# Performance work log

Hardware: AMD Instinct MI355X
Metric: run time of the kernel (lower is better)

Reference implementation:

```python
import jax, jax.numpy as jnp
import numpy as np

N_CORES = 64
N_QUBITS = 1024
QEMB = 256
N_EDGES = 448
BATCH = 512
NN_DIMS = (256, 512, 512, 256)


def setup_inputs() -> dict:
    key = jax.random.key(0)
    ks = jax.random.split(key, 12)
    inp = {
        "core_allocs": jax.random.randint(ks[0], (BATCH, N_QUBITS), 0, N_CORES, dtype=jnp.int32),
        "qubit_embs": jax.random.normal(ks[1], (N_QUBITS, QEMB), dtype=jnp.float32),
        "dummy_qubit_emb": jax.random.normal(ks[2], (QEMB,), dtype=jnp.float32),
        "edge_index": jax.random.randint(ks[3], (2, N_EDGES), 0, N_CORES, dtype=jnp.int32),
        "edge_weight": jax.random.uniform(ks[4], (N_EDGES,), dtype=jnp.float32),
        "W1": jax.random.normal(ks[5], (NN_DIMS[0], NN_DIMS[1]), dtype=jnp.float32) * 0.05,
        "b1": jax.random.normal(ks[6], (NN_DIMS[1],), dtype=jnp.float32) * 0.05,
        "W2": jax.random.normal(ks[7], (NN_DIMS[1], NN_DIMS[2]), dtype=jnp.float32) * 0.05,
        "b2": jax.random.normal(ks[8], (NN_DIMS[2],), dtype=jnp.float32) * 0.05,
        "W3": jax.random.normal(ks[9], (NN_DIMS[2], NN_DIMS[3]), dtype=jnp.float32) * 0.05,
        "b3": jax.random.normal(ks[10], (NN_DIMS[3],), dtype=jnp.float32) * 0.05,
    }
    return inp


def _gcn_norm(edge_index, edge_weight):
    # PyG gcn_norm: add self loops (weight 1), symmetric D^{-1/2} A D^{-1/2}.
    self_idx = jnp.arange(N_CORES, dtype=edge_index.dtype)
    row = jnp.concatenate([edge_index[0], self_idx])
    col = jnp.concatenate([edge_index[1], self_idx])
    w = jnp.concatenate([edge_weight, jnp.ones((N_CORES,), edge_weight.dtype)])
    deg = jax.ops.segment_sum(w, col, num_segments=N_CORES)  # degree at targets
    dinv = jnp.where(deg > 0, deg ** -0.5, 0.0)
    norm = dinv[row] * w * dinv[col]
    return row, col, norm


def reference(core_allocs, qubit_embs, dummy_qubit_emb, edge_index, edge_weight,
              W1, b1, W2, b2, W3, b3):
    # ---- unmixedCoreEmbs, vectorized: per-core max over assigned qubit embs,
    # dummy emb always included (cores never at capacity) ----
    def pool(alloc):  # alloc: [n_qubits] -> [n_cores, qemb]
        seg = jax.ops.segment_max(qubit_embs, alloc, num_segments=N_CORES)
        return jnp.maximum(seg, dummy_qubit_emb)  # also fixes -inf empty cores

    x = jax.vmap(pool)(core_allocs)  # [B, n_cores, qemb]

    # ---- GCNConv stack (same graph replicated per batch element) ----
    row, col, norm = _gcn_norm(edge_index, edge_weight)

    def gcn_layer(h, W, b):
        hw = h @ W  # [B, C, d_out]
        msg = hw[:, row, :] * norm[None, :, None]  # gather sources, scale
        agg = jnp.zeros((h.shape[0], N_CORES, W.shape[1]), hw.dtype).at[:, col, :].add(msg)
        return jax.nn.relu(agg + b)

    x = gcn_layer(x, W1, b1)
    x = gcn_layer(x, W2, b2)
    x = gcn_layer(x, W3, b3)
    return x  # [B, n_cores, nn_dims[-1]] (original returns this split per batch element)
```

## Files before the change

kernel.cpp:

```cpp
#include <hip/hip_runtime.h>
#include <type_traits>

typedef __attribute__((ext_vector_type(8))) short short8;
typedef __attribute__((ext_vector_type(4))) short short4v;
typedef __attribute__((ext_vector_type(4))) float f32x4;
typedef unsigned short u16;
typedef unsigned int u32;

#define N_EDGES 448

#define WS_ADJA 0
#define WS_ADJB 4096
#define WS_W1   8192
#define WS_W2   139264
#define WS_W3   401408
#define WS_DUM  532480
#define WS_B1   (WS_DUM + 256)
#define WS_B2   (WS_DUM + 768)
#define WS_B3   (WS_DUM + 1280)
#define WS_QE   534528
#define WS_FLAG 796672

__device__ __forceinline__ float bf2f(u16 v) {
    u32 u = ((u32)v) << 16;
    return __builtin_bit_cast(float, u);
}
__device__ __forceinline__ u16 f2bf(float f) {
    u32 u = __builtin_bit_cast(u32, f);
    u32 r = u + 0x7FFFu + ((u >> 16) & 1u);
    return (u16)(r >> 16);
}
__device__ __forceinline__ float ldf(const void* p, int idx, u32 isf32) {
    return isf32 ? ((const float*)p)[idx] : bf2f(((const u16*)p)[idx]);
}

__global__ __launch_bounds__(512) void prep(
    const int* __restrict__ eidx, const void* __restrict__ ew,
    const void* __restrict__ qembs, const void* __restrict__ dummy,
    const void* __restrict__ W1, const void* __restrict__ b1,
    const void* __restrict__ W2, const void* __restrict__ b2,
    const void* __restrict__ W3, const void* __restrict__ b3,
    u16* __restrict__ ws) {
    const int t = threadIdx.x, bb = blockIdx.x;
    __shared__ u32 s_isf;
    if (t < 64) {
        const u16* qs = (const u16*)qembs;
        int c = 0;
#pragma unroll
        for (int j = 0; j < 4; j++) {
            u16 v = qs[(t * 4 + j) * 2];
            u32 e = (v >> 7) & 0xFF;
            c += (e >= 100 && e <= 134) ? 1 : 0;
        }
#pragma unroll
        for (int off = 32; off > 0; off >>= 1) c += __shfl_down(c, off, 64);
        if (t == 0) s_isf = (c < 128) ? 1u : 0u;
    }
    __syncthreads();
    const u32 isf32 = s_isf;

    if (t < 128) {
        const int bw = bb * 2 + (t >> 6);
        const int tl = t & 63;
        const void* src;
        int N, K32, dst, nt, kk;
        if (bw < 256)      { src = W1; N = 512; K32 = 8;  dst = WS_W1; nt = bw / 8;          kk = bw % 8; }
        else if (bw < 768) { src = W2; N = 512; K32 = 16; dst = WS_W2; nt = (bw - 256) / 16; kk = (bw - 256) % 16; }
        else               { src = W3; N = 256; K32 = 16; dst = WS_W3; nt = (bw - 768) / 16; kk = (bw - 768) % 16; }
        const int col = nt * 16 + (tl & 15);
        const int krow = kk * 32 + (tl >> 4) * 8;
        u16 v[8];
#pragma unroll
        for (int j = 0; j < 8; j++) v[j] = f2bf(ldf(src, (krow + j) * N + col, isf32));
        u16* o = ws + dst + (nt * K32 + kk) * 512 + tl * 8;
#pragma unroll
        for (int j = 0; j < 8; j++) o[j] = v[j];
    }
    if (t >= 256) {
        const int base = bb * 512 + (t - 256) * 2;
        ws[WS_QE + base]     = f2bf(ldf(qembs, base, isf32));
        ws[WS_QE + base + 1] = f2bf(ldf(qembs, base + 1, isf32));
    }
    if (bb == 1) {
#pragma unroll
        for (int j = 0; j < 4; j++) {
            int i = t + j * 512;
            if (i < 1792) {
                float v;
                if (i < 256)       v = ldf(dummy, i, isf32);
                else if (i < 768)  v = ldf(b1, i - 256, isf32);
                else if (i < 1280) v = ldf(b2, i - 768, isf32);
                else               v = ldf(b3, i - 1280, isf32);
                ws[WS_DUM + i] = f2bf(v);
            }
        }
    }
    if (bb == 0) {
        __shared__ float A[4096];
        __shared__ float deg[64];
        __shared__ float dinv[64];
        __shared__ int er[N_EDGES];
        __shared__ int ec[N_EDGES];
        __shared__ float ewf[N_EDGES];
        if (t < N_EDGES) {
            er[t] = eidx[t];
            ec[t] = eidx[N_EDGES + t];
            ewf[t] = ldf(ew, t, isf32);
        }
        if (t < 64) deg[t] = 1.0f;
        for (int i = t; i < 4096; i += 512) A[i] = 0.f;
        __syncthreads();
        if (t < N_EDGES) atomicAdd(&deg[ec[t]], ewf[t]);
        __syncthreads();
        if (t < 64) dinv[t] = 1.0f / sqrtf(deg[t]);
        __syncthreads();
        if (t < N_EDGES) atomicAdd(&A[ec[t] * 64 + er[t]], dinv[er[t]] * ewf[t] * dinv[ec[t]]);
        __syncthreads();
        if (t < 64) A[t * 64 + t] += dinv[t] * dinv[t];
        __syncthreads();
        for (int i = t; i < 4096; i += 512) {
            int chunk = i >> 9, m = (i >> 3) & 63, j = i & 7;
            ws[WS_ADJA + i] = f2bf(A[m * 64 + chunk * 8 + j]);
        }
        for (int i = t; i < 4096; i += 512) {
            int chunk = i >> 9, l = (i >> 3) & 63, j = i & 7;
            int ntc = chunk >> 1, kk = chunk & 1;
            int k = kk * 32 + (l >> 4) * 8 + j;
            int c2 = ntc * 16 + (l & 15);
            ws[WS_ADJB + i] = f2bf(A[c2 * 64 + k]);
        }
        if (t == 0) *(u32*)(ws + WS_FLAG) = isf32;
    }
}

__global__ __launch_bounds__(1024, 8) void fused(
    const int* __restrict__ allocs, const u16* __restrict__ ws,
    void* __restrict__ out) {

    __shared__ __align__(16) u16 H[64 * 512];

    const int t = threadIdx.x, bb = blockIdx.x;
    const int wave = t >> 6, lane = t & 63, quad = lane >> 4, nl = lane & 15;

    {
        int* LIST = (int*)H + 8192;
        int* CNT  = LIST + 1024;
        int* SST  = CNT + 64;
        int* WOF  = SST + 64;
        if (t < 64) CNT[t] = 0;
        __syncthreads();
        const int myc = allocs[bb * 1024 + t];
        atomicAdd(&CNT[myc], 1);
        __syncthreads();
        if (t < 64) {
            int v = CNT[t], s = v;
#pragma unroll
            for (int off = 1; off < 64; off <<= 1) {
                int u = __shfl_up(s, off, 64);
                if (t >= off) s += u;
            }
            SST[t] = s - v;
            WOF[t] = s - v;
        }
        __syncthreads();
        {
            int pos = atomicAdd(&WOF[myc], 1);
            LIST[pos] = t;
        }
        __syncthreads();
        const int half = lane >> 5, sl = lane & 31;
        const u16* wsq = ws + WS_QE;
        for (int i = 0; i < 4; i++) {
            const int c = wave * 4 + i;
            const int L = CNT[c], S = SST[c];
            float vm[8];
#pragma unroll
            for (int k = 0; k < 8; k++) vm[k] = bf2f(ws[WS_DUM + sl * 8 + k]);
            for (int j = half; j < L; j += 2) {
                int q = LIST[S + j];
                uint4 r = *(const uint4*)(wsq + q * 256 + sl * 8);
                vm[0] = fmaxf(vm[0], bf2f((u16)(r.x & 0xffff)));
                vm[1] = fmaxf(vm[1], bf2f((u16)(r.x >> 16)));
                vm[2] = fmaxf(vm[2], bf2f((u16)(r.y & 0xffff)));
                vm[3] = fmaxf(vm[3], bf2f((u16)(r.y >> 16)));
                vm[4] = fmaxf(vm[4], bf2f((u16)(r.z & 0xffff)));
                vm[5] = fmaxf(vm[5], bf2f((u16)(r.z >> 16)));
                vm[6] = fmaxf(vm[6], bf2f((u16)(r.w & 0xffff)));
                vm[7] = fmaxf(vm[7], bf2f((u16)(r.w >> 16)));
            }
            short8 p;
#pragma unroll
            for (int k = 0; k < 8; k++) {
                float o = __shfl_xor(vm[k], 32, 64);
                p[k] = (short)f2bf(fmaxf(vm[k], o));
            }
            if (half == 0) *(short8*)(H + sl * 512 + c * 8) = p;
        }
    }
    __syncthreads();

    auto layerT = [&](auto K32c, const u16* __restrict__ W, const u16* __restrict__ bias) {
        constexpr int K32 = decltype(K32c)::value;
        const int s0 = wave * 2;
        u16* scr = H + (wave * 4 + 2) * 512;
        f32x4 acc[2][4];
#pragma unroll
        for (int s = 0; s < 2; s++)
#pragma unroll
            for (int rt = 0; rt < 4; rt++) acc[s][rt] = f32x4{0.f, 0.f, 0.f, 0.f};
#pragma unroll
        for (int kk = 0; kk < K32; kk++) {
            short8 a[4], bch[2];
#pragma unroll
            for (int rt = 0; rt < 4; rt++)
                a[rt] = *(const short8*)(H + (kk * 4 + quad) * 512 + (rt * 16 + nl) * 8);
#pragma unroll
            for (int s = 0; s < 2; s++)
                bch[s] = *(const short8*)(W + ((s0 + s) * K32 + kk) * 512 + lane * 8);
#pragma unroll
            for (int s = 0; s < 2; s++)
#pragma unroll
                for (int rt = 0; rt < 4; rt++)
                    acc[s][rt] = __builtin_amdgcn_mfma_f32_16x16x32_bf16(a[rt], bch[s], acc[s][rt], 0, 0, 0);
        }
        __syncthreads();
#pragma unroll
        for (int s = 0; s < 2; s++) {
            const int nt = s0 + s;
            f32x4 agg[4];
#pragma unroll
            for (int ntc = 0; ntc < 4; ntc++) agg[ntc] = f32x4{0.f, 0.f, 0.f, 0.f};
#pragma unroll
            for (int h = 0; h < 2; h++) {
#pragma unroll
                for (int r2 = 0; r2 < 2; r2++) {
                    f32x4 v = acc[s][2 * h + r2];
                    short4v p;
#pragma unroll
                    for (int rr = 0; rr < 4; rr++) p[rr] = (short)f2bf(v[rr]);
                    *(short4v*)(scr + nl * 40 + r2 * 16 + quad * 4) = p;
                }
                short8 hwf = *(const short8*)(scr + nl * 40 + quad * 8);
#pragma unroll
                for (int ntc = 0; ntc < 4; ntc++) {
                    short8 adjB = *(const short8*)(ws + WS_ADJB + (ntc * 2 + h) * 512 + lane * 8);
                    agg[ntc] = __builtin_amdgcn_mfma_f32_16x16x32_bf16(hwf, adjB, agg[ntc], 0, 0, 0);
                }
            }
            float bv[4];
#pragma unroll
            for (int rr = 0; rr < 4; rr++) bv[rr] = bf2f(bias[nt * 16 + quad * 4 + rr]);
#pragma unroll
            for (int ntc = 0; ntc < 4; ntc++) {
                short4v p;
#pragma unroll
                for (int rr = 0; rr < 4; rr++)
                    p[rr] = (short)f2bf(fmaxf(agg[ntc][rr] + bv[rr], 0.f));
                *(short4v*)(H + (nt * 2 + (quad >> 1)) * 512 + (ntc * 16 + nl) * 8 + (quad & 1) * 4) = p;
            }
        }
        __syncthreads();
    };

    auto layer3 = [&](const u16* __restrict__ W) {
        const int nt = wave;
        u16* scr = H + 16384 + wave * 640;
        f32x4 acc[4];
#pragma unroll
        for (int rt = 0; rt < 4; rt++) acc[rt] = f32x4{0.f, 0.f, 0.f, 0.f};
#pragma unroll
        for (int kk = 0; kk < 16; kk++) {
            short8 a[4];
#pragma unroll
            for (int rt = 0; rt < 4; rt++)
                a[rt] = *(const short8*)(H + (kk * 4 + quad) * 512 + (rt * 16 + nl) * 8);
            short8 bch = *(const short8*)(W + (nt * 16 + kk) * 512 + lane * 8);
#pragma unroll
            for (int rt = 0; rt < 4; rt++)
                acc[rt] = __builtin_amdgcn_mfma_f32_16x16x32_bf16(a[rt], bch, acc[rt], 0, 0, 0);
        }
        __syncthreads();
#pragma unroll
        for (int h = 0; h < 2; h++) {
#pragma unroll
            for (int r2 = 0; r2 < 2; r2++) {
                f32x4 v = acc[2 * h + r2];
                short4v p;
#pragma unroll
                for (int rr = 0; rr < 4; rr++) p[rr] = (short)f2bf(v[rr]);
                *(short4v*)(scr + nl * 40 + r2 * 16 + quad * 4) = p;
            }
            short8 hwf = *(const short8*)(scr + nl * 40 + quad * 8);
            *(short8*)(H + (nt * 2 + h) * 512 + lane * 8) = hwf;
        }
        __syncthreads();
    };

    auto finalOut = [&]() {
        const u32 isf32 = *(const u32*)(ws + WS_FLAG);
        const int rt2 = wave & 3, nt0 = (wave >> 2) * 4;
        short8 aA[2];
#pragma unroll
        for (int h = 0; h < 2; h++)
            aA[h] = *(const short8*)(ws + WS_ADJA + (h * 4 + quad) * 512 + (rt2 * 16 + nl) * 8);
        f32x4 accv[4];
#pragma unroll
        for (int ni = 0; ni < 4; ni++) {
            const int nt = nt0 + ni;
            short8 b0v = *(const short8*)(H + (nt * 2 + 0) * 512 + lane * 8);
            short8 b1v = *(const short8*)(H + (nt * 2 + 1) * 512 + lane * 8);
            f32x4 a = f32x4{0.f, 0.f, 0.f, 0.f};
            a = __builtin_amdgcn_mfma_f32_16x16x32_bf16(aA[0], b0v, a, 0, 0, 0);
            a = __builtin_amdgcn_mfma_f32_16x16x32_bf16(aA[1], b1v, a, 0, 0, 0);
            accv[ni] = a;
        }
        __syncthreads();
        float* Hf = (float*)H;
#pragma unroll
        for (int ni = 0; ni < 4; ni++) {
            const int n = (nt0 + ni) * 16 + nl;
            const float bv = bf2f(ws[WS_B3 + n]);
#pragma unroll
            for (int rr = 0; rr < 4; rr++) {
                const int m2 = rt2 * 16 + quad * 4 + rr;
                Hf[m2 * 256 + n] = fmaxf(accv[ni][rr] + bv, 0.f);
            }
        }
        __syncthreads();
        if (isf32) {
            float4* outv = (float4*)((float*)out + (size_t)bb * 16384);
            const float4* Hv = (const float4*)Hf;
#pragma unroll
            for (int p4 = 0; p4 < 4; p4++) outv[p4 * 1024 + t] = Hv[p4 * 1024 + t];
        } else {
            u16* outu = (u16*)out + (size_t)bb * 16384;
#pragma unroll
            for (int p4 = 0; p4 < 4; p4++) {
                const int idx = (p4 * 1024 + t) * 4;
                float4 v = *(const float4*)(Hf + idx);
                short4v pk;
                pk[0] = (short)f2bf(v.x); pk[1] = (short)f2bf(v.y);
                pk[2] = (short)f2bf(v.z); pk[3] = (short)f2bf(v.w);
                *(short4v*)(outu + idx) = pk;
            }
        }
    };

    layerT(std::integral_constant<int, 8>{},  ws + WS_W1, ws + WS_B1);
    layerT(std::integral_constant<int, 16>{}, ws + WS_W2, ws + WS_B2);
    layer3(ws + WS_W3);
    finalOut();
}

extern "C" void kernel_launch(void* const* d_in, const int* in_sizes, int n_in,
                              void* d_out, int out_size, void* d_ws, size_t ws_size,
                              hipStream_t stream) {
    const int* allocs = (const int*)d_in[0];
    const void* qembs = d_in[1];
    const void* dummy = d_in[2];
    const int* eidx   = (const int*)d_in[3];
    const void* ew    = d_in[4];
    const void* W1 = d_in[5];
    const void* b1 = d_in[6];
    const void* W2 = d_in[7];
    const void* b2 = d_in[8];
    const void* W3 = d_in[9];
    const void* b3 = d_in[10];
    u16* ws = (u16*)d_ws;

    prep<<<512, 512, 0, stream>>>(eidx, ew, qembs, dummy, W1, b1, W2, b2, W3, b3, ws);
    fused<<<512, 1024, 0, stream>>>(allocs, ws, d_out);
}
```

Measured before the change: 173.0 us.

## Halve fused block to 512 threads, doubling per-wave GEMM tiles; use cheaper bf16 rounding

The fused kernel now runs 512 threads per block instead of 1024, and each wave covers twice as many output tiles in every stage: pooling over 8 cores, 4 n-tiles in the first two GCN layers, 2 in layer3, and 8 in the final output. This raises per-wave register reuse of the A fragments loaded from LDS and cuts barrier participants. The price is fewer waves for latency hiding and more accumulator registers. Float-to-bf16 conversion also switches to round-half-up without ties-to-even, which saves a few ALU ops but can differ slightly in rounding.

```diff
diff --git a/kernel.cpp b/kernel.cpp
--- a/kernel.cpp
+++ b/kernel.cpp
@@ -29,6 +29,10 @@
     u32 u = __builtin_bit_cast(u32, f);
     u32 r = u + 0x7FFFu + ((u >> 16) & 1u);
     return (u16)(r >> 16);
+}
+__device__ __forceinline__ u16 f2bf_fast(float f) {
+    u32 u = __builtin_bit_cast(u32, f);
+    return (u16)((u + 0x8000u) >> 16);
 }
 __device__ __forceinline__ float ldf(const void* p, int idx, u32 isf32) {
     return isf32 ? ((const float*)p)[idx] : bf2f(((const u16*)p)[idx]);
@@ -133,7 +137,7 @@
     }
 }
 
-__global__ __launch_bounds__(1024, 8) void fused(
+__global__ __launch_bounds__(512, 4) void fused(
     const int* __restrict__ allocs, const u16* __restrict__ ws,
     void* __restrict__ out) {
 
@@ -149,8 +153,10 @@
         int* WOF  = SST + 64;
         if (t < 64) CNT[t] = 0;
         __syncthreads();
-        const int myc = allocs[bb * 1024 + t];
-        atomicAdd(&CNT[myc], 1);
+        const int c1 = allocs[bb * 1024 + t];
+        const int c2 = allocs[bb * 1024 + 512 + t];
+        atomicAdd(&CNT[c1], 1);
+        atomicAdd(&CNT[c2], 1);
         __syncthreads();
         if (t < 64) {
             int v = CNT[t], s = v;
@@ -164,14 +170,14 @@
         }
         __syncthreads();
         {
-            int pos = atomicAdd(&WOF[myc], 1);
-            LIST[pos] = t;
+            int p1 = atomicAdd(&WOF[c1], 1); LIST[p1] = t;
+            int p2 = atomicAdd(&WOF[c2], 1); LIST[p2] = 512 + t;
         }
         __syncthreads();
         const int half = lane >> 5, sl = lane & 31;
         const u16* wsq = ws + WS_QE;
-        for (int i = 0; i < 4; i++) {
-            const int c = wave * 4 + i;
+        for (int i = 0; i < 8; i++) {
+            const int c = wave * 8 + i;
             const int L = CNT[c], S = SST[c];
             float vm[8];
 #pragma unroll
@@ -192,7 +198,7 @@
 #pragma unroll
             for (int k = 0; k < 8; k++) {
                 float o = __shfl_xor(vm[k], 32, 64);
-                p[k] = (short)f2bf(fmaxf(vm[k], o));
+                p[k] = (short)f2bf_fast(fmaxf(vm[k], o));
             }
             if (half == 0) *(short8*)(H + sl * 512 + c * 8) = p;
         }
@@ -201,31 +207,31 @@
 
     auto layerT = [&](auto K32c, const u16* __restrict__ W, const u16* __restrict__ bias) {
         constexpr int K32 = decltype(K32c)::value;
-        const int s0 = wave * 2;
-        u16* scr = H + (wave * 4 + 2) * 512;
-        f32x4 acc[2][4];
-#pragma unroll
-        for (int s = 0; s < 2; s++)
+        const int s0 = wave * 4;
+        u16* scr = H + (wave * 8 + 6) * 512;
+        f32x4 acc[4][4];
+#pragma unroll
+        for (int s = 0; s < 4; s++)
 #pragma unroll
             for (int rt = 0; rt < 4; rt++) acc[s][rt] = f32x4{0.f, 0.f, 0.f, 0.f};
 #pragma unroll
         for (int kk = 0; kk < K32; kk++) {
-            short8 a[4], bch[2];
+            short8 a[4], bch[4];
 #pragma unroll
             for (int rt = 0; rt < 4; rt++)
                 a[rt] = *(const short8*)(H + (kk * 4 + quad) * 512 + (rt * 16 + nl) * 8);
 #pragma unroll
-            for (int s = 0; s < 2; s++)
+            for (int s = 0; s < 4; s++)
                 bch[s] = *(const short8*)(W + ((s0 + s) * K32 + kk) * 512 + lane * 8);
 #pragma unroll
-            for (int s = 0; s < 2; s++)
+            for (int s = 0; s < 4; s++)
 #pragma unroll
                 for (int rt = 0; rt < 4; rt++)
                     acc[s][rt] = __builtin_amdgcn_mfma_f32_16x16x32_bf16(a[rt], bch[s], acc[s][rt], 0, 0, 0);
         }
         __syncthreads();
 #pragma unroll
-        for (int s = 0; s < 2; s++) {
+        for (int s = 0; s < 4; s++) {
             const int nt = s0 + s;
             f32x4 agg[4];
 #pragma unroll
@@ -237,7 +243,7 @@
                     f32x4 v = acc[s][2 * h + r2];
                     short4v p;
 #pragma unroll
-                    for (int rr = 0; rr < 4; rr++) p[rr] = (short)f2bf(v[rr]);
+                    for (int rr = 0; rr < 4; rr++) p[rr] = (short)f2bf_fast(v[rr]);
                     *(short4v*)(scr + nl * 40 + r2 * 16 + quad * 4) = p;
                 }
                 short8 hwf = *(const short8*)(scr + nl * 40 + quad * 8);
@@ -255,7 +261,7 @@
                 short4v p;
 #pragma unroll
                 for (int rr = 0; rr < 4; rr++)
-                    p[rr] = (short)f2bf(fmaxf(agg[ntc][rr] + bv[rr], 0.f));
+                    p[rr] = (short)f2bf_fast(fmaxf(agg[ntc][rr] + bv[rr], 0.f));
                 *(short4v*)(H + (nt * 2 + (quad >> 1)) * 512 + (ntc * 16 + nl) * 8 + (quad & 1) * 4) = p;
             }
         }
@@ -263,49 +269,59 @@
     };
 
     auto layer3 = [&](const u16* __restrict__ W) {
-        const int nt = wave;
+        const int s0 = wave * 2;
         u16* scr = H + 16384 + wave * 640;
-        f32x4 acc[4];
-#pragma unroll
-        for (int rt = 0; rt < 4; rt++) acc[rt] = f32x4{0.f, 0.f, 0.f, 0.f};
+        f32x4 acc[2][4];
+#pragma unroll
+        for (int s = 0; s < 2; s++)
+#pragma unroll
+            for (int rt = 0; rt < 4; rt++) acc[s][rt] = f32x4{0.f, 0.f, 0.f, 0.f};
 #pragma unroll
         for (int kk = 0; kk < 16; kk++) {
-            short8 a[4];
+            short8 a[4], bch[2];
 #pragma unroll
             for (int rt = 0; rt < 4; rt++)
                 a[rt] = *(const short8*)(H + (kk * 4 + quad) * 512 + (rt * 16 + nl) * 8);
-            short8 bch = *(const short8*)(W + (nt * 16 + kk) * 512 + lane * 8);
-#pragma unroll
-            for (int rt = 0; rt < 4; rt++)
-                acc[rt] = __builtin_amdgcn_mfma_f32_16x16x32_bf16(a[rt], bch, acc[rt], 0, 0, 0);
-        }
-        __syncthreads();
-#pragma unroll
-        for (int h = 0; h < 2; h++) {
-#pragma unroll
-            for (int r2 = 0; r2 < 2; r2++) {
-                f32x4 v = acc[2 * h + r2];
-                short4v p;
-#pragma unroll
-                for (int rr = 0; rr < 4; rr++) p[rr] = (short)f2bf(v[rr]);
-                *(short4v*)(scr + nl * 40 + r2 * 16 + quad * 4) = p;
-            }
-            short8 hwf = *(const short8*)(scr + nl * 40 + quad * 8);
-            *(short8*)(H + (nt * 2 + h) * 512 + lane * 8) = hwf;
+#pragma unroll
+            for (int s = 0; s < 2; s++)
+                bch[s] = *(const short8*)(W + ((s0 + s) * 16 + kk) * 512 + lane * 8);
+#pragma unroll
+            for (int s = 0; s < 2; s++)
+#pragma unroll
+                for (int rt = 0; rt < 4; rt++)
+                    acc[s][rt] = __builtin_amdgcn_mfma_f32_16x16x32_bf16(a[rt], bch[s], acc[s][rt], 0, 0, 0);
+        }
+        __syncthreads();
+#pragma unroll
+        for (int s = 0; s < 2; s++) {
+            const int nt = s0 + s;
+#pragma unroll
+            for (int h = 0; h < 2; h++) {
+#pragma unroll
+                for (int r2 = 0; r2 < 2; r2++) {
+                    f32x4 v = acc[s][2 * h + r2];
+                    short4v p;
+#pragma unroll
+                    for (int rr = 0; rr < 4; rr++) p[rr] = (short)f2bf_fast(v[rr]);
+                    *(short4v*)(scr + nl * 40 + r2 * 16 + quad * 4) = p;
+                }
+                short8 hwf = *(const short8*)(scr + nl * 40 + quad * 8);
+                *(short8*)(H + (nt * 2 + h) * 512 + lane * 8) = hwf;
+            }
         }
         __syncthreads();
     };
 
     auto finalOut = [&]() {
         const u32 isf32 = *(const u32*)(ws + WS_FLAG);
-        const int rt2 = wave & 3, nt0 = (wave >> 2) * 4;
+        const int rt2 = wave & 3, nt0 = (wave >> 2) * 8;
         short8 aA[2];
 #pragma unroll
         for (int h = 0; h < 2; h++)
             aA[h] = *(const short8*)(ws + WS_ADJA + (h * 4 + quad) * 512 + (rt2 * 16 + nl) * 8);
-        f32x4 accv[4];
-#pragma unroll
-        for (int ni = 0; ni < 4; ni++) {
+        f32x4 accv[8];
+#pragma unroll
+        for (int ni = 0; ni < 8; ni++) {
             const int nt = nt0 + ni;
             short8 b0v = *(const short8*)(H + (nt * 2 + 0) * 512 + lane * 8);
             short8 b1v = *(const short8*)(H + (nt * 2 + 1) * 512 + lane * 8);
@@ -317,7 +333,7 @@
         __syncthreads();
         float* Hf = (float*)H;
 #pragma unroll
-        for (int ni = 0; ni < 4; ni++) {
+        for (int ni = 0; ni < 8; ni++) {
             const int n = (nt0 + ni) * 16 + nl;
             const float bv = bf2f(ws[WS_B3 + n]);
 #pragma unroll
@@ -331,16 +347,16 @@
             float4* outv = (float4*)((float*)out + (size_t)bb * 16384);
             const float4* Hv = (const float4*)Hf;
 #pragma unroll
-            for (int p4 = 0; p4 < 4; p4++) outv[p4 * 1024 + t] = Hv[p4 * 1024 + t];
+            for (int p4 = 0; p4 < 8; p4++) outv[p4 * 512 + t] = Hv[p4 * 512 + t];
         } else {
             u16* outu = (u16*)out + (size_t)bb * 16384;
 #pragma unroll
-            for (int p4 = 0; p4 < 4; p4++) {
-                const int idx = (p4 * 1024 + t) * 4;
+            for (int p4 = 0; p4 < 8; p4++) {
+                const int idx = (p4 * 512 + t) * 4;
                 float4 v = *(const float4*)(Hf + idx);
                 short4v pk;
-                pk[0] = (short)f2bf(v.x); pk[1] = (short)f2bf(v.y);
-                pk[2] = (short)f2bf(v.z); pk[3] = (short)f2bf(v.w);
+                pk[0] = (short)f2bf_fast(v.x); pk[1] = (short)f2bf_fast(v.y);
+                pk[2] = (short)f2bf_fast(v.z); pk[3] = (short)f2bf_fast(v.w);
                 *(short4v*)(outu + idx) = pk;
             }
         }
@@ -369,5 +385,5 @@
     u16* ws = (u16*)d_ws;
 
     prep<<<512, 512, 0, stream>>>(eidx, ew, qembs, dummy, W1, b1, W2, b2, W3, b3, ws);
-    fused<<<512, 1024, 0, stream>>>(allocs, ws, d_out);
-}
+    fused<<<512, 512, 0, stream>>>(allocs, ws, d_out);
+}
```

New measurement: 163.2 us. -5.7%, faster.

## Merge prep and fused kernels into one persistent kernel with grid barrier

Applied to the files above, without the earlier changes.

Folds the weight/embedding preprocessing kernel and the main GCN kernel into a single launch of 256 blocks, separated by a software grid-wide barrier on a global counter reset by a memset. Each block now processes two batch elements, ping-pongs activations between two LDS buffers so some __syncthreads are removed, and uses a cheaper round-to-nearest bf16 conversion. The pooling gather is reworked to one wave per core reading 4 elements per lane. The goal is to cut launch overhead and the extra syncs. The trade-offs are a spin barrier that assumes all 256 blocks are co-resident, halved grid parallelism, a memset call, and slightly different rounding.

```diff
diff --git a/kernel.cpp b/kernel.cpp
--- a/kernel.cpp
+++ b/kernel.cpp
@@ -19,7 +19,7 @@
 #define WS_B2   (WS_DUM + 768)
 #define WS_B3   (WS_DUM + 1280)
 #define WS_QE   534528
-#define WS_FLAG 796672
+#define WS_BAR  796672
 
 __device__ __forceinline__ float bf2f(u16 v) {
     u32 u = ((u32)v) << 16;
@@ -30,19 +30,30 @@
     u32 r = u + 0x7FFFu + ((u >> 16) & 1u);
     return (u16)(r >> 16);
 }
+__device__ __forceinline__ u16 f2bf_fast(float f) {
+    u32 u = __builtin_bit_cast(u32, f);
+    return (u16)((u + 0x8000u) >> 16);
+}
 __device__ __forceinline__ float ldf(const void* p, int idx, u32 isf32) {
     return isf32 ? ((const float*)p)[idx] : bf2f(((const u16*)p)[idx]);
 }
 
-__global__ __launch_bounds__(512) void prep(
-    const int* __restrict__ eidx, const void* __restrict__ ew,
-    const void* __restrict__ qembs, const void* __restrict__ dummy,
+__global__ __launch_bounds__(1024, 4) void mega(
+    const int* __restrict__ allocs, const void* __restrict__ qembs,
+    const void* __restrict__ dummy, const int* __restrict__ eidx,
+    const void* __restrict__ ew,
     const void* __restrict__ W1, const void* __restrict__ b1,
     const void* __restrict__ W2, const void* __restrict__ b2,
     const void* __restrict__ W3, const void* __restrict__ b3,
-    u16* __restrict__ ws) {
+    u16* __restrict__ ws, void* __restrict__ out) {
+
+    __shared__ __align__(16) u16 BUF0[64 * 512];
+    __shared__ __align__(16) u16 BUF1[64 * 512];
+    __shared__ u32 s_isf;
+
     const int t = threadIdx.x, bb = blockIdx.x;
-    __shared__ u32 s_isf;
+    const int wave = t >> 6, lane = t & 63, quad = lane >> 4, nl = lane & 15;
+
     if (t < 64) {
         const u16* qs = (const u16*)qembs;
         int c = 0;
@@ -59,8 +70,8 @@
     __syncthreads();
     const u32 isf32 = s_isf;
 
-    if (t < 128) {
-        const int bw = bb * 2 + (t >> 6);
+    if (t < 256) {
+        const int bw = bb * 4 + (t >> 6);
         const int tl = t & 63;
         const void* src;
         int N, K32, dst, nt, kk;
@@ -76,15 +87,15 @@
 #pragma unroll
         for (int j = 0; j < 8; j++) o[j] = v[j];
     }
-    if (t >= 256) {
-        const int base = bb * 512 + (t - 256) * 2;
+    if (t >= 512) {
+        const int base = bb * 1024 + (t - 512) * 2;
         ws[WS_QE + base]     = f2bf(ldf(qembs, base, isf32));
         ws[WS_QE + base + 1] = f2bf(ldf(qembs, base + 1, isf32));
     }
     if (bb == 1) {
 #pragma unroll
-        for (int j = 0; j < 4; j++) {
-            int i = t + j * 512;
+        for (int j = 0; j < 2; j++) {
+            int i = t + j * 1024;
             if (i < 1792) {
                 float v;
                 if (i < 256)       v = ldf(dummy, i, isf32);
@@ -96,19 +107,19 @@
         }
     }
     if (bb == 0) {
-        __shared__ float A[4096];
-        __shared__ float deg[64];
-        __shared__ float dinv[64];
-        __shared__ int er[N_EDGES];
-        __shared__ int ec[N_EDGES];
-        __shared__ float ewf[N_EDGES];
+        float* A    = (float*)BUF0;
+        int*   er   = (int*)BUF0 + 4096;
+        int*   ec   = (int*)BUF0 + 4544;
+        float* ewf  = (float*)BUF0 + 4992;
+        float* deg  = (float*)BUF1;
+        float* dinv = (float*)BUF1 + 64;
         if (t < N_EDGES) {
             er[t] = eidx[t];
             ec[t] = eidx[N_EDGES + t];
             ewf[t] = ldf(ew, t, isf32);
         }
         if (t < 64) deg[t] = 1.0f;
-        for (int i = t; i < 4096; i += 512) A[i] = 0.f;
+        for (int i = t; i < 4096; i += 1024) A[i] = 0.f;
         __syncthreads();
         if (t < N_EDGES) atomicAdd(&deg[ec[t]], ewf[t]);
         __syncthreads();
@@ -118,238 +129,238 @@
         __syncthreads();
         if (t < 64) A[t * 64 + t] += dinv[t] * dinv[t];
         __syncthreads();
-        for (int i = t; i < 4096; i += 512) {
+        for (int i = t; i < 4096; i += 1024) {
             int chunk = i >> 9, m = (i >> 3) & 63, j = i & 7;
             ws[WS_ADJA + i] = f2bf(A[m * 64 + chunk * 8 + j]);
         }
-        for (int i = t; i < 4096; i += 512) {
+        for (int i = t; i < 4096; i += 1024) {
             int chunk = i >> 9, l = (i >> 3) & 63, j = i & 7;
             int ntc = chunk >> 1, kk = chunk & 1;
             int k = kk * 32 + (l >> 4) * 8 + j;
             int c2 = ntc * 16 + (l & 15);
             ws[WS_ADJB + i] = f2bf(A[c2 * 64 + k]);
         }
-        if (t == 0) *(u32*)(ws + WS_FLAG) = isf32;
-    }
-}
-
-__global__ __launch_bounds__(1024, 8) void fused(
-    const int* __restrict__ allocs, const u16* __restrict__ ws,
-    void* __restrict__ out) {
-
-    __shared__ __align__(16) u16 H[64 * 512];
-
-    const int t = threadIdx.x, bb = blockIdx.x;
-    const int wave = t >> 6, lane = t & 63, quad = lane >> 4, nl = lane & 15;
-
+    }
+
+    __syncthreads();
+    __threadfence();
     {
-        int* LIST = (int*)H + 8192;
-        int* CNT  = LIST + 1024;
-        int* SST  = CNT + 64;
-        int* WOF  = SST + 64;
-        if (t < 64) CNT[t] = 0;
-        __syncthreads();
-        const int myc = allocs[bb * 1024 + t];
-        atomicAdd(&CNT[myc], 1);
-        __syncthreads();
-        if (t < 64) {
-            int v = CNT[t], s = v;
-#pragma unroll
-            for (int off = 1; off < 64; off <<= 1) {
-                int u = __shfl_up(s, off, 64);
-                if (t >= off) s += u;
-            }
-            SST[t] = s - v;
-            WOF[t] = s - v;
-        }
-        __syncthreads();
+        u32* cnt = (u32*)(ws + WS_BAR);
+        if (t == 0) {
+            __hip_atomic_fetch_add(cnt, 1u, __ATOMIC_RELEASE, __HIP_MEMORY_SCOPE_AGENT);
+            long spins = 0;
+            while (__hip_atomic_load(cnt, __ATOMIC_ACQUIRE, __HIP_MEMORY_SCOPE_AGENT) < 256u
+                   && ++spins < 200000000L) { }
+        }
+        __syncthreads();
+        __threadfence();
+    }
+
+    for (int e = 0; e < 2; e++) {
+        const int elem = bb * 2 + e;
+
         {
-            int pos = atomicAdd(&WOF[myc], 1);
-            LIST[pos] = t;
-        }
-        __syncthreads();
-        const int half = lane >> 5, sl = lane & 31;
-        const u16* wsq = ws + WS_QE;
-        for (int i = 0; i < 4; i++) {
-            const int c = wave * 4 + i;
-            const int L = CNT[c], S = SST[c];
-            float vm[8];
-#pragma unroll
-            for (int k = 0; k < 8; k++) vm[k] = bf2f(ws[WS_DUM + sl * 8 + k]);
-            for (int j = half; j < L; j += 2) {
-                int q = LIST[S + j];
-                uint4 r = *(const uint4*)(wsq + q * 256 + sl * 8);
-                vm[0] = fmaxf(vm[0], bf2f((u16)(r.x & 0xffff)));
-                vm[1] = fmaxf(vm[1], bf2f((u16)(r.x >> 16)));
-                vm[2] = fmaxf(vm[2], bf2f((u16)(r.y & 0xffff)));
-                vm[3] = fmaxf(vm[3], bf2f((u16)(r.y >> 16)));
-                vm[4] = fmaxf(vm[4], bf2f((u16)(r.z & 0xffff)));
-                vm[5] = fmaxf(vm[5], bf2f((u16)(r.z >> 16)));
-                vm[6] = fmaxf(vm[6], bf2f((u16)(r.w & 0xffff)));
-                vm[7] = fmaxf(vm[7], bf2f((u16)(r.w >> 16)));
-            }
-            short8 p;
-#pragma unroll
-            for (int k = 0; k < 8; k++) {
-                float o = __shfl_xor(vm[k], 32, 64);
-                p[k] = (short)f2bf(fmaxf(vm[k], o));
-            }
-            if (half == 0) *(short8*)(H + sl * 512 + c * 8) = p;
-        }
-    }
-    __syncthreads();
-
-    auto layerT = [&](auto K32c, const u16* __restrict__ W, const u16* __restrict__ bias) {
-        constexpr int K32 = decltype(K32c)::value;
-        const int s0 = wave * 2;
-        u16* scr = H + (wave * 4 + 2) * 512;
-        f32x4 acc[2][4];
-#pragma unroll
-        for (int s = 0; s < 2; s++)
-#pragma unroll
-            for (int rt = 0; rt < 4; rt++) acc[s][rt] = f32x4{0.f, 0.f, 0.f, 0.f};
-#pragma unroll
-        for (int kk = 0; kk < K32; kk++) {
-            short8 a[4], bch[2];
-#pragma unroll
-            for (int rt = 0; rt < 4; rt++)
-                a[rt] = *(const short8*)(H + (kk * 4 + quad) * 512 + (rt * 16 + nl) * 8);
+            int* LIST = (int*)BUF1;
+            int* CNT  = LIST + 1024;
+            int* SST  = CNT + 64;
+            int* WOF  = SST + 64;
+            if (t < 64) CNT[t] = 0;
+            __syncthreads();
+            const int myc = allocs[elem * 1024 + t];
+            atomicAdd(&CNT[myc], 1);
+            __syncthreads();
+            if (t < 64) {
+                int v = CNT[t], s = v;
+#pragma unroll
+                for (int off = 1; off < 64; off <<= 1) {
+                    int u = __shfl_up(s, off, 64);
+                    if (t >= off) s += u;
+                }
+                SST[t] = s - v;
+                WOF[t] = s - v;
+            }
+            __syncthreads();
+            {
+                int pos = atomicAdd(&WOF[myc], 1);
+                LIST[pos] = t;
+            }
+            __syncthreads();
+            float dums[4];
+#pragma unroll
+            for (int jj = 0; jj < 4; jj++) dums[jj] = bf2f(ws[WS_DUM + lane * 4 + jj]);
+            const u16* wsq = ws + WS_QE;
+            for (int i = 0; i < 4; i++) {
+                const int c = wave * 4 + i;
+                const int L = CNT[c], S = SST[c];
+                float vm0 = dums[0], vm1 = dums[1], vm2 = dums[2], vm3 = dums[3];
+                for (int j = 0; j < L; j++) {
+                    int q = LIST[S + j];
+                    uint2 r = *(const uint2*)(wsq + q * 256 + lane * 4);
+                    vm0 = fmaxf(vm0, bf2f((u16)(r.x & 0xffff)));
+                    vm1 = fmaxf(vm1, bf2f((u16)(r.x >> 16)));
+                    vm2 = fmaxf(vm2, bf2f((u16)(r.y & 0xffff)));
+                    vm3 = fmaxf(vm3, bf2f((u16)(r.y >> 16)));
+                }
+                short4v p;
+                p[0] = (short)f2bf_fast(vm0);
+                p[1] = (short)f2bf_fast(vm1);
+                p[2] = (short)f2bf_fast(vm2);
+                p[3] = (short)f2bf_fast(vm3);
+                *(short4v*)(BUF0 + (lane >> 1) * 512 + c * 8 + (lane & 1) * 4) = p;
+            }
+        }
+        __syncthreads();
+
+        auto layerT = [&](auto K32c, const u16* __restrict__ W, const u16* __restrict__ bias,
+                          const u16* __restrict__ IN, u16* __restrict__ OUT) {
+            constexpr int K32 = decltype(K32c)::value;
+            const int s0 = wave * 2;
+            u16* scr = OUT + (wave * 4 + 2) * 512;
+            f32x4 acc[2][4];
 #pragma unroll
             for (int s = 0; s < 2; s++)
-                bch[s] = *(const short8*)(W + ((s0 + s) * K32 + kk) * 512 + lane * 8);
-#pragma unroll
-            for (int s = 0; s < 2; s++)
+#pragma unroll
+                for (int rt = 0; rt < 4; rt++) acc[s][rt] = f32x4{0.f, 0.f, 0.f, 0.f};
+#pragma unroll
+            for (int kk = 0; kk < K32; kk++) {
+                short8 a[4], bch[2];
 #pragma unroll
                 for (int rt = 0; rt < 4; rt++)
-                    acc[s][rt] = __builtin_amdgcn_mfma_f32_16x16x32_bf16(a[rt], bch[s], acc[s][rt], 0, 0, 0);
-        }
-        __syncthreads();
-#pragma unroll
-        for (int s = 0; s < 2; s++) {
-            const int nt = s0 + s;
-            f32x4 agg[4];
-#pragma unroll
-            for (int ntc = 0; ntc < 4; ntc++) agg[ntc] = f32x4{0.f, 0.f, 0.f, 0.f};
+                    a[rt] = *(const short8*)(IN + (kk * 4 + quad) * 512 + (rt * 16 + nl) * 8);
+#pragma unroll
+                for (int s = 0; s < 2; s++)
+                    bch[s] = *(const short8*)(W + ((s0 + s) * K32 + kk) * 512 + lane * 8);
+#pragma unroll
+                for (int s = 0; s < 2; s++)
+#pragma unroll
+                    for (int rt = 0; rt < 4; rt++)
+                        acc[s][rt] = __builtin_amdgcn_mfma_f32_16x16x32_bf16(a[rt], bch[s], acc[s][rt], 0, 0, 0);
+            }
+#pragma unroll
+            for (int s = 0; s < 2; s++) {
+                const int nt = s0 + s;
+                f32x4 agg[4];
+#pragma unroll
+                for (int ntc = 0; ntc < 4; ntc++) agg[ntc] = f32x4{0.f, 0.f, 0.f, 0.f};
+#pragma unroll
+                for (int h = 0; h < 2; h++) {
+#pragma unroll
+                    for (int r2 = 0; r2 < 2; r2++) {
+                        f32x4 v = acc[s][2 * h + r2];
+                        short4v p;
+#pragma unroll
+                        for (int rr = 0; rr < 4; rr++) p[rr] = (short)f2bf_fast(v[rr]);
+                        *(short4v*)(scr + nl * 40 + r2 * 16 + quad * 4) = p;
+                    }
+                    short8 hwf = *(const short8*)(scr + nl * 40 + quad * 8);
+#pragma unroll
+                    for (int ntc = 0; ntc < 4; ntc++) {
+                        short8 adjB = *(const short8*)(ws + WS_ADJB + (ntc * 2 + h) * 512 + lane * 8);
+                        agg[ntc] = __builtin_amdgcn_mfma_f32_16x16x32_bf16(hwf, adjB, agg[ntc], 0, 0, 0);
+                    }
+                }
+                float bv[4];
+#pragma unroll
+                for (int rr = 0; rr < 4; rr++) bv[rr] = bf2f(bias[nt * 16 + quad * 4 + rr]);
+#pragma unroll
+                for (int ntc = 0; ntc < 4; ntc++) {
+                    short4v p;
+#pragma unroll
+                    for (int rr = 0; rr < 4; rr++)
+                        p[rr] = (short)f2bf_fast(fmaxf(agg[ntc][rr] + bv[rr], 0.f));
+                    *(short4v*)(OUT + (nt * 2 + (quad >> 1)) * 512 + (ntc * 16 + nl) * 8 + (quad & 1) * 4) = p;
+                }
+            }
+            __syncthreads();
+        };
+
+        auto layer3 = [&](const u16* __restrict__ W, const u16* __restrict__ IN,
+                          u16* __restrict__ OUT) {
+            const int nt = wave;
+            u16* scr = OUT + 16384 + wave * 640;
+            f32x4 acc[4];
+#pragma unroll
+            for (int rt = 0; rt < 4; rt++) acc[rt] = f32x4{0.f, 0.f, 0.f, 0.f};
+#pragma unroll
+            for (int kk = 0; kk < 16; kk++) {
+                short8 a[4];
+#pragma unroll
+                for (int rt = 0; rt < 4; rt++)
+                    a[rt] = *(const short8*)(IN + (kk * 4 + quad) * 512 + (rt * 16 + nl) * 8);
+                short8 bch = *(const short8*)(W + (nt * 16 + kk) * 512 + lane * 8);
+#pragma unroll
+                for (int rt = 0; rt < 4; rt++)
+                    acc[rt] = __builtin_amdgcn_mfma_f32_16x16x32_bf16(a[rt], bch, acc[rt], 0, 0, 0);
+            }
 #pragma unroll
             for (int h = 0; h < 2; h++) {
 #pragma unroll
                 for (int r2 = 0; r2 < 2; r2++) {
-                    f32x4 v = acc[s][2 * h + r2];
+                    f32x4 v = acc[2 * h + r2];
                     short4v p;
 #pragma unroll
-                    for (int rr = 0; rr < 4; rr++) p[rr] = (short)f2bf(v[rr]);
+                    for (int rr = 0; rr < 4; rr++) p[rr] = (short)f2bf_fast(v[rr]);
                     *(short4v*)(scr + nl * 40 + r2 * 16 + quad * 4) = p;
                 }
                 short8 hwf = *(const short8*)(scr + nl * 40 + quad * 8);
-#pragma unroll
-                for (int ntc = 0; ntc < 4; ntc++) {
-                    short8 adjB = *(const short8*)(ws + WS_ADJB + (ntc * 2 + h) * 512 + lane * 8);
-                    agg[ntc] = __builtin_amdgcn_mfma_f32_16x16x32_bf16(hwf, adjB, agg[ntc], 0, 0, 0);
-                }
-            }
-            float bv[4];
-#pragma unroll
-            for (int rr = 0; rr < 4; rr++) bv[rr] = bf2f(bias[nt * 16 + quad * 4 + rr]);
-#pragma unroll
-            for (int ntc = 0; ntc < 4; ntc++) {
-                short4v p;
-#pragma unroll
-                for (int rr = 0; rr < 4; rr++)
-                    p[rr] = (short)f2bf(fmaxf(agg[ntc][rr] + bv[rr], 0.f));
-                *(short4v*)(H + (nt * 2 + (quad >> 1)) * 512 + (ntc * 16 + nl) * 8 + (quad & 1) * 4) = p;
-            }
-        }
-        __syncthreads();
-    };
-
-    auto layer3 = [&](const u16* __restrict__ W) {
-        const int nt = wave;
-        u16* scr = H + 16384 + wave * 640;
-        f32x4 acc[4];
-#pragma unroll
-        for (int rt = 0; rt < 4; rt++) acc[rt] = f32x4{0.f, 0.f, 0.f, 0.f};
-#pragma unroll
-        for (int kk = 0; kk < 16; kk++) {
-            short8 a[4];
-#pragma unroll
-            for (int rt = 0; rt < 4; rt++)
-                a[rt] = *(const short8*)(H + (kk * 4 + quad) * 512 + (rt * 16 + nl) * 8);
-            short8 bch = *(const short8*)(W + (nt * 16 + kk) * 512 + lane * 8);
-#pragma unroll
-            for (int rt = 0; rt < 4; rt++)
-                acc[rt] = __builtin_amdgcn_mfma_f32_16x16x32_bf16(a[rt], bch, acc[rt], 0, 0, 0);
-        }
-        __syncthreads();
-#pragma unroll
-        for (int h = 0; h < 2; h++) {
-#pragma unroll
-            for (int r2 = 0; r2 < 2; r2++) {
-                f32x4 v = acc[2 * h + r2];
-                short4v p;
-#pragma unroll
-                for (int rr = 0; rr < 4; rr++) p[rr] = (short)f2bf(v[rr]);
-                *(short4v*)(scr + nl * 40 + r2 * 16 + quad * 4) = p;
-            }
-            short8 hwf = *(const short8*)(scr + nl * 40 + quad * 8);
-            *(short8*)(H + (nt * 2 + h) * 512 + lane * 8) = hwf;
-        }
-        __syncthreads();
-    };
-
-    auto finalOut = [&]() {
-        const u32 isf32 = *(const u32*)(ws + WS_FLAG);
-        const int rt2 = wave & 3, nt0 = (wave >> 2) * 4;
-        short8 aA[2];
-#pragma unroll
-        for (int h = 0; h < 2; h++)
-            aA[h] = *(const short8*)(ws + WS_ADJA + (h * 4 + quad) * 512 + (rt2 * 16 + nl) * 8);
-        f32x4 accv[4];
-#pragma unroll
-        for (int ni = 0; ni < 4; ni++) {
-            const int nt = nt0 + ni;
-            short8 b0v = *(const short8*)(H + (nt * 2 + 0) * 512 + lane * 8);
-            short8 b1v = *(const short8*)(H + (nt * 2 + 1) * 512 + lane * 8);
-            f32x4 a = f32x4{0.f, 0.f, 0.f, 0.f};
-            a = __builtin_amdgcn_mfma_f32_16x16x32_bf16(aA[0], b0v, a, 0, 0, 0);
-            a = __builtin_amdgcn_mfma_f32_16x16x32_bf16(aA[1], b1v, a, 0, 0, 0);
-            accv[ni] = a;
-        }
-        __syncthreads();
-        float* Hf = (float*)H;
-#pragma unroll
-        for (int ni = 0; ni < 4; ni++) {
-            const int n = (nt0 + ni) * 16 + nl;
-            const float bv = bf2f(ws[WS_B3 + n]);
-#pragma unroll
-            for (int rr = 0; rr < 4; rr++) {
-                const int m2 = rt2 * 16 + quad * 4 + rr;
-                Hf[m2 * 256 + n] = fmaxf(accv[ni][rr] + bv, 0.f);
-            }
-        }
-        __syncthreads();
-        if (isf32) {
-            float4* outv = (float4*)((float*)out + (size_t)bb * 16384);
-            const float4* Hv = (const float4*)Hf;
-#pragma unroll
-            for (int p4 = 0; p4 < 4; p4++) outv[p4 * 1024 + t] = Hv[p4 * 1024 + t];
-        } else {
-            u16* outu = (u16*)out + (size_t)bb * 16384;
-#pragma unroll
-            for (int p4 = 0; p4 < 4; p4++) {
-                const int idx = (p4 * 1024 + t) * 4;
-                float4 v = *(const float4*)(Hf + idx);
-                short4v pk;
-                pk[0] = (short)f2bf(v.x); pk[1] = (short)f2bf(v.y);
-                pk[2] = (short)f2bf(v.z); pk[3] = (short)f2bf(v.w);
-                *(short4v*)(outu + idx) = pk;
-            }
-        }
-    };
-
-    layerT(std::integral_constant<int, 8>{},  ws + WS_W1, ws + WS_B1);
-    layerT(std::integral_constant<int, 16>{}, ws + WS_W2, ws + WS_B2);
-    layer3(ws + WS_W3);
-    finalOut();
+                *(short8*)(OUT + (nt * 2 + h) * 512 + lane * 8) = hwf;
+            }
+            __syncthreads();
+        };
+
+        layerT(std::integral_constant<int, 8>{},  ws + WS_W1, ws + WS_B1, BUF0, BUF1);
+        layerT(std::integral_constant<int, 16>{}, ws + WS_W2, ws + WS_B2, BUF1, BUF0);
+        layer3(ws + WS_W3, BUF0, BUF1);
+
+        {
+            const int rt2 = wave & 3, nt0 = (wave >> 2) * 4;
+            short8 aA[2];
+#pragma unroll
+            for (int h = 0; h < 2; h++)
+                aA[h] = *(const short8*)(ws + WS_ADJA + (h * 4 + quad) * 512 + (rt2 * 16 + nl) * 8);
+            f32x4 accv[4];
+#pragma unroll
+            for (int ni = 0; ni < 4; ni++) {
+                const int nt = nt0 + ni;
+                short8 b0v = *(const short8*)(BUF1 + (nt * 2 + 0) * 512 + lane * 8);
+                short8 b1v = *(const short8*)(BUF1 + (nt * 2 + 1) * 512 + lane * 8);
+                f32x4 a = f32x4{0.f, 0.f, 0.f, 0.f};
+                a = __builtin_amdgcn_mfma_f32_16x16x32_bf16(aA[0], b0v, a, 0, 0, 0);
+                a = __builtin_amdgcn_mfma_f32_16x16x32_bf16(aA[1], b1v, a, 0, 0, 0);
+                accv[ni] = a;
+            }
+            float* Hf = (float*)BUF0;
+#pragma unroll
+            for (int ni = 0; ni < 4; ni++) {
+                const int n = (nt0 + ni) * 16 + nl;
+                const float bv = bf2f(ws[WS_B3 + n]);
+#pragma unroll
+                for (int rr = 0; rr < 4; rr++) {
+                    const int m2 = rt2 * 16 + quad * 4 + rr;
+                    Hf[m2 * 256 + n] = fmaxf(accv[ni][rr] + bv, 0.f);
+                }
+            }
+            __syncthreads();
+            if (isf32) {
+                float4* outv = (float4*)((float*)out + (size_t)elem * 16384);
+                const float4* Hv = (const float4*)Hf;
+#pragma unroll
+                for (int p4 = 0; p4 < 4; p4++) outv[p4 * 1024 + t] = Hv[p4 * 1024 + t];
+            } else {
+                u16* outu = (u16*)out + (size_t)elem * 16384;
+#pragma unroll
+                for (int p4 = 0; p4 < 4; p4++) {
+                    const int idx = (p4 * 1024 + t) * 4;
+                    float4 v = *(const float4*)(Hf + idx);
+                    short4v pk;
+                    pk[0] = (short)f2bf_fast(v.x); pk[1] = (short)f2bf_fast(v.y);
+                    pk[2] = (short)f2bf_fast(v.z); pk[3] = (short)f2bf_fast(v.w);
+                    *(short4v*)(outu + idx) = pk;
+                }
+            }
+        }
+        __syncthreads();
+    }
 }
 
 extern "C" void kernel_launch(void* const* d_in, const int* in_sizes, int n_in,
@@ -368,6 +379,7 @@
     const void* b3 = d_in[10];
     u16* ws = (u16*)d_ws;
 
-    prep<<<512, 512, 0, stream>>>(eidx, ew, qembs, dummy, W1, b1, W2, b2, W3, b3, ws);
-    fused<<<512, 1024, 0, stream>>>(allocs, ws, d_out);
-}
+    hipMemsetAsync((char*)d_ws + (size_t)WS_BAR * 2, 0, 64, stream);
+    mega<<<256, 1024, 0, stream>>>(allocs, qembs, dummy, eidx, ew,
+                                   W1, b1, W2, b2, W3, b3, ws, d_out);
+}
```

New measurement: 382.9 us. 2.21x slower.
